# Kernel optimization log

Measured on AMD Instinct MI355X. Metric: run time of the kernel, lower is better.

Reference implementation:

```python
import jax, jax.numpy as jnp
import numpy as np

S, SM, B, D, H, NHEAD = 1024, 1024, 4, 1024, 2048, 16
EPS = 1e-5


def layer_norm(x, g, b):
    mu = jnp.mean(x, axis=-1, keepdims=True)
    var = jnp.var(x, axis=-1, keepdims=True)
    return (x - mu) * jax.lax.rsqrt(var + EPS) * g + b


def mha(q_in, k_in, v_in, w_in, b_in, w_out, b_out):
    # q_in: [Sq,B,D], k_in/v_in: [Sk,B,D]; torch nn.MultiheadAttention math (eval)
    Sq, Bn, Dn = q_in.shape
    Sk = k_in.shape[0]
    hd = Dn // NHEAD
    wq, wk, wv = jnp.split(w_in, 3, axis=0)
    bq, bk, bv = jnp.split(b_in, 3)
    q = (q_in @ wq.T + bq) * (hd ** -0.5)
    k = k_in @ wk.T + bk
    v = v_in @ wv.T + bv
    rs = lambda x, L: x.reshape(L, Bn, NHEAD, hd).transpose(1, 2, 0, 3)  # [B,h,L,hd]
    qh, kh, vh = rs(q, Sq), rs(k, Sk), rs(v, Sk)
    att = jax.nn.softmax(jnp.einsum('bhqd,bhkd->bhqk', qh, kh), axis=-1)
    o = jnp.einsum('bhqk,bhkd->bhqd', att, vh).transpose(2, 0, 1, 3).reshape(Sq, Bn, Dn)
    return o @ w_out.T + b_out


def sru(x, w, v, b):
    # SRU cell with input projection (n_in != n_out -> k=4): candidate, f, r, highway
    Ssz, Bsz, _ = x.shape
    U = (x @ w).reshape(Ssz, Bsz, 4, H)  # [S,B,4,H]
    vf, vr = v[0], v[1]
    bf, br = b[0], b[1]

    def step(c, u):
        xc, fp, rp, xh = u[:, 0], u[:, 1], u[:, 2], u[:, 3]
        f = jax.nn.sigmoid(fp + vf * c + bf)
        r = jax.nn.sigmoid(rp + vr * c + br)
        c2 = f * c + (1.0 - f) * xc
        h = r * c2 + (1.0 - r) * xh
        return c2, h

    c0 = jnp.zeros((Bsz, H), x.dtype)
    _, hs = jax.lax.scan(step, c0, U)
    return hs  # [S,B,H]


def setup_inputs():
    key = jax.random.key(0)
    ks = jax.random.split(key, 12)
    n = lambda k, shp, sc=0.02: jax.random.normal(k, shp, dtype=jnp.float32) * sc
    return dict(
        tgt=n(ks[0], (S, B, D), 1.0),
        memory=n(ks[1], (SM, B, D), 1.0),
        sa_w_in=n(ks[2], (3 * D, D)), sa_b_in=jnp.zeros((3 * D,)),
        sa_w_out=n(ks[3], (D, D)), sa_b_out=jnp.zeros((D,)),
        ca_w_in=n(ks[4], (3 * D, D)), ca_b_in=jnp.zeros((3 * D,)),
        ca_w_out=n(ks[5], (D, D)), ca_b_out=jnp.zeros((D,)),
        sru_w=n(ks[6], (D, 4 * H)), sru_v=n(ks[7], (2, H)), sru_b=jnp.zeros((2, H)),
        lin2_w=n(ks[8], (D, H)), lin2_b=jnp.zeros((D,)),
        ln1_g=jnp.ones((D,)), ln1_b=jnp.zeros((D,)),
        ln2_g=jnp.ones((D,)), ln2_b=jnp.zeros((D,)),
        ln3_g=jnp.ones((D,)), ln3_b=jnp.zeros((D,)),
    )


def reference(tgt, memory, sa_w_in, sa_b_in, sa_w_out, sa_b_out,
              ca_w_in, ca_b_in, ca_w_out, ca_b_out,
              sru_w, sru_v, sru_b, lin2_w, lin2_b,
              ln1_g, ln1_b, ln2_g, ln2_b, ln3_g, ln3_b):
    # dropout layers are identity in eval mode
    t2 = mha(tgt, tgt, tgt, sa_w_in, sa_b_in, sa_w_out, sa_b_out)
    t = layer_norm(tgt + t2, ln1_g, ln1_b)
    t2 = mha(t, memory, memory, ca_w_in, ca_b_in, ca_w_out, ca_b_out)
    t = layer_norm(t + t2, ln2_g, ln2_b)
    h = sru(t, sru_w, sru_v, sru_b)
    t2 = h @ lin2_w.T + lin2_b
    t = layer_norm(t + t2, ln3_g, ln3_b)
    return t
```

## Files before the change

kernel.cpp:

```cpp
#include <hip/hip_runtime.h>
#include <hip/hip_bf16.h>

typedef __bf16 bf16;
typedef bf16 bf16x8 __attribute__((ext_vector_type(8)));
typedef bf16 bf16x4 __attribute__((ext_vector_type(4)));
typedef float f32x4 __attribute__((ext_vector_type(4)));

#define MFMA16(a, b, c) __builtin_amdgcn_mfma_f32_16x16x32_bf16((a), (b), (c), 0, 0, 0)

__device__ __forceinline__ void gl_lds16(const void* g, void* l) {
    __builtin_amdgcn_global_load_lds((const __attribute__((address_space(1))) void*)g,
                                     (__attribute__((address_space(3))) void*)l, 16, 0, 0);
}

__global__ __launch_bounds__(256) void k_detect(const void* __restrict__ src, int* __restrict__ flag) {
    __shared__ int cnt;
    if (threadIdx.x == 0) cnt = 0;
    __syncthreads();
    const unsigned int* w = (const unsigned int*)src;
    int local = 0;
    for (int i = threadIdx.x; i < 4096; i += 256) {
        unsigned int e = (w[i] >> 7) & 0xFF;
        local += (e > 100 && e < 150) ? 1 : 0;
    }
    atomicAdd(&cnt, local);
    __syncthreads();
    if (threadIdx.x == 0) *flag = (cnt > 2048) ? 1 : 0;
}

struct BigSegs {
    const void* src[6];
    bf16* dst[6];
    int cum[7];
};
__global__ __launch_bounds__(256) void k_norm_big(const int* __restrict__ flag, BigSegs s) {
    if (*flag) return;
    int seg = 0;
#pragma unroll
    for (int t = 0; t < 5; t++) seg += (blockIdx.x >= s.cum[t + 1]) ? 1 : 0;
    int i = (blockIdx.x - s.cum[seg]) * 256 + threadIdx.x;
    const float* fs = (const float*)s.src[seg] + (size_t)i * 8;
    bf16x8 o;
#pragma unroll
    for (int j = 0; j < 8; j++) o[j] = (bf16)fs[j];
    ((bf16x8*)s.dst[seg])[i] = o;
}

struct SmallSegs {
    const void* src[13];
    bf16* dst[13];
    int n8[13];
};
__global__ __launch_bounds__(256) void k_norm_multi(const int* __restrict__ flag, SmallSegs s) {
    int seg = blockIdx.x;
    const void* sp = s.src[seg];
    bf16* dp = s.dst[seg];
    int n = s.n8[seg];
    int f = *flag;
    for (int i = threadIdx.x; i < n; i += 256) {
        if (f) {
            ((bf16x8*)dp)[i] = ((const bf16x8*)sp)[i];
        } else {
            const float* fs = (const float*)sp + (size_t)i * 8;
            bf16x8 o;
#pragma unroll
            for (int j = 0; j < 8; j++) o[j] = (bf16)fs[j];
            ((bf16x8*)dp)[i] = o;
        }
    }
}

__global__ __launch_bounds__(256) void k_cvt(const int* __restrict__ flag, const void* __restrict__ in,
                                             bf16* __restrict__ outb) {
    if (*flag) return;
    size_t i = (size_t)blockIdx.x * 256 + threadIdx.x;
    f32x4 a = ((const f32x4*)in)[i * 2];
    f32x4 b = ((const f32x4*)in)[i * 2 + 1];
    bf16x8 v;
#pragma unroll
    for (int j = 0; j < 4; j++) { v[j] = (bf16)a[j]; v[4 + j] = (bf16)b[j]; }
    ((bf16x8*)outb)[i] = v;
}

__global__ __launch_bounds__(256) void k_transpose(const int* __restrict__ flag, const void* __restrict__ in,
                                                   bf16* __restrict__ out, int R, int C) {
    __shared__ __align__(16) bf16 t[64][72];
    int tid = threadIdx.x;
    int c0 = blockIdx.x * 64, r0 = blockIdx.y * 64;
#pragma unroll
    for (int i = 0; i < 2; i++) {
        int idx = tid + i * 256;
        int r = idx >> 3, ch = idx & 7;
        size_t base = (size_t)(r0 + r) * C + c0 + ch * 8;
        bf16x8 v;
        if (*flag) {
            v = *(const bf16x8*)((const bf16*)in + base);
        } else {
            const float* f = (const float*)in + base;
            f32x4 x = *(const f32x4*)f, y = *(const f32x4*)(f + 4);
#pragma unroll
            for (int j = 0; j < 4; j++) { v[j] = (bf16)x[j]; v[4 + j] = (bf16)y[j]; }
        }
        *(bf16x8*)&t[r][ch * 8] = v;
    }
    __syncthreads();
    int nbase = c0 & 2047, joff = c0 >> 11;
#pragma unroll
    for (int i = 0; i < 2; i++) {
        int idx = tid + i * 256;
        int cr = idx >> 3, ch = idx & 7;
        bf16x8 v;
#pragma unroll
        for (int j = 0; j < 8; j++) v[j] = t[ch * 8 + j][cr];
        int np = (nbase + cr) * 4 + joff;
        *(bf16x8*)(out + (size_t)np * R + r0 + ch * 8) = v;
    }
}

__global__ __launch_bounds__(256) void k_vtr(const bf16* __restrict__ in, int ldv, bf16* __restrict__ out) {
    int nt = blockIdx.x, st = blockIdx.y, b = blockIdx.z;
    __shared__ __align__(16) bf16 t[64][72];
    int tid = threadIdx.x;
#pragma unroll
    for (int i = 0; i < 2; i++) {
        int idx = tid + i * 256;
        int r = idx >> 3, ch = idx & 7;
        bf16x8 v = *(const bf16x8*)(in + (size_t)((st * 64 + r) * 4 + b) * ldv + nt * 64 + ch * 8);
        *(bf16x8*)&t[r][ch * 8] = v;
    }
    __syncthreads();
#pragma unroll
    for (int i = 0; i < 2; i++) {
        int idx = tid + i * 256;
        int dr = idx >> 3, ch = idx & 7;
        bf16x8 v;
#pragma unroll
        for (int j = 0; j < 8; j++) v[j] = t[ch * 8 + j][dr];
        *(bf16x8*)(out + (size_t)(b * 1024 + nt * 64 + dr) * 1024 + st * 64 + ch * 8) = v;
    }
}

__device__ __forceinline__ int swzB(int r, int byteInRow) {
    return r * 128 + (byteInRow ^ ((r & 7) << 4));
}

template <int BM, bool USCAT>
__global__ __launch_bounds__(256) void k_gemm(
    const int* __restrict__ flagp,
    const bf16* __restrict__ A, const bf16* __restrict__ Aalt, int lda,
    const bf16* __restrict__ W, const bf16* __restrict__ Walt, int ldw,
    const bf16* __restrict__ bias,
    float* __restrict__ Cf, bf16* __restrict__ Cb, int ldc,
    int K, int scale_end, float scale) {
    constexpr int MI = BM / 32;
    __shared__ __align__(16) char Asm[BM * 128];
    __shared__ __align__(16) char Bsm[128 * 128];
    if (*flagp) {
        if (Aalt) A = Aalt;
        if (Walt) W = Walt;
    }
    int tid = threadIdx.x, w = tid >> 6, l = tid & 63, lg = l >> 4, lm = l & 15;
    int wm = w >> 1, wn = w & 1;
    int m0 = blockIdx.y * BM, n0 = blockIdx.x * 128;

    f32x4 acc[MI][4] = {};

    for (int k0 = 0; k0 < K; k0 += 64) {
#pragma unroll
        for (int i = 0; i < BM / 32; i++) {
            int r = i * 32 + w * 8 + (l >> 3);
            int gs = (l & 7) ^ (r & 7);
            gl_lds16(A + (size_t)(m0 + r) * lda + k0 + gs * 8,
                     Asm + (i * 32 + w * 8) * 128);
        }
#pragma unroll
        for (int i = 0; i < 4; i++) {
            int r = i * 32 + w * 8 + (l >> 3);
            int gs = (l & 7) ^ (r & 7);
            gl_lds16(W + (size_t)(n0 + r) * ldw + k0 + gs * 8,
                     Bsm + (i * 32 + w * 8) * 128);
        }
        __syncthreads();
#pragma unroll
        for (int kh = 0; kh < 2; kh++) {
            bf16x8 af[MI], bfr[4];
#pragma unroll
            for (int i = 0; i < MI; i++)
                af[i] = *(const bf16x8*)(Asm + swzB(wm * (BM / 2) + i * 16 + lm, kh * 64 + lg * 16));
#pragma unroll
            for (int j = 0; j < 4; j++)
                bfr[j] = *(const bf16x8*)(Bsm + swzB(wn * 64 + j * 16 + lm, kh * 64 + lg * 16));
#pragma unroll
            for (int i = 0; i < MI; i++)
#pragma unroll
                for (int j = 0; j < 4; j++)
                    acc[i][j] = MFMA16(af[i], bfr[j], acc[i][j]);
        }
        __syncthreads();
    }
    if constexpr (USCAT) {
        bf16* lsA = (bf16*)Asm;
        bf16* lsB = (bf16*)Bsm;
#pragma unroll
        for (int j = 0; j < 4; j++) {
            int cl = wn * 16 + j * 4 + (lm >> 2);
            int g = lm & 3;
            bf16* ls = (g < 2) ? lsA : lsB;
            int g01 = g & 1;
#pragma unroll
            for (int i = 0; i < MI; i++) {
                int slb = wm * 16 + i * 4 + lg;
                int boff = (slb * 2 + g01) * 2;
                int swz = boff ^ ((cl & 7) << 4);
#pragma unroll
                for (int r = 0; r < 4; r++) {
                    float v = acc[i][j][r];
                    *(bf16*)((char*)ls + (r * 32 + cl) * 128 + swz) = (bf16)v;
                }
            }
        }
        __syncthreads();
        int buf = tid >> 7, bb = (tid >> 5) & 3, cl = tid & 31;
        const char* ls = (buf == 0) ? (const char*)lsA : (const char*)lsB;
        bf16* dstbase = (buf == 0) ? Cb : (bf16*)Cf;
        int ch = bb * 2048 + (n0 >> 2) + cl;
        size_t gbase = (size_t)ch * 2048 + (size_t)(m0 >> 2) * 2;
        const char* src = ls + (bb * 32 + cl) * 128;
#pragma unroll
        for (int q = 0; q < 8; q++) {
            int pq = (q * 16) ^ ((cl & 7) << 4);
            *(bf16x8*)(dstbase + gbase + q * 8) = *(const bf16x8*)(src + pq);
        }
    } else {
#pragma unroll
        for (int j = 0; j < 4; j++) {
            int col = n0 + wn * 64 + j * 16 + lm;
            float bv = bias ? (float)bias[col] : 0.f;
            float sc = (col < scale_end) ? scale : 1.f;
#pragma unroll
            for (int i = 0; i < MI; i++) {
                int row = m0 + wm * (BM / 2) + i * 16 + lg * 4;
#pragma unroll
                for (int r = 0; r < 4; r++) {
                    float v = (acc[i][j][r] + bv) * sc;
                    size_t idx = (size_t)(row + r) * ldc + col;
                    if (Cf) Cf[idx] = v;
                    if (Cb) Cb[idx] = (bf16)v;
                }
            }
        }
    }
}

__device__ __forceinline__ int swz2(int row, int byteInRow) {
    return row * 128 + (byteInRow ^ ((row & 7) << 4));
}
__device__ __forceinline__ int swzP(int row, int byteInRow) {
    return row * 128 + (byteInRow ^ ((row & 3) << 4) ^ (((row >> 2) & 1) << 6));
}

__global__ __launch_bounds__(256) void k_attn(
    const bf16* __restrict__ Qp, const bf16* __restrict__ Kp, const bf16* __restrict__ Vt,
    int ldq, int ldk, bf16* __restrict__ Op) {
    int h = blockIdx.x & 15, b = blockIdx.x >> 4, qblk = blockIdx.y;
    int tid = threadIdx.x, w = tid >> 6, l = tid & 63, lg = l >> 4, lm = l & 15;
    int r0 = tid >> 3, ch = tid & 7;

    __shared__ __align__(16) char Ksm[2][64 * 128];
    __shared__ __align__(16) char Vsm[2][64 * 128];
    __shared__ __align__(16) char Psm[4][32 * 128];

    bf16x8 qf[2][2];
#pragma unroll
    for (int u = 0; u < 2; u++) {
        int qrow = qblk * 128 + w * 32 + u * 16 + lm;
#pragma unroll
        for (int kk = 0; kk < 2; kk++)
            qf[u][kk] = *(const bf16x8*)(Qp + (size_t)(qrow * 4 + b) * ldq + h * 64 + kk * 32 + lg * 8);
    }

    const bf16* vbase = Vt + (size_t)(b * 1024 + h * 64) * 1024;

    bf16x8 kreg[2], vreg[2];
#pragma unroll
    for (int p = 0; p < 2; p++) {
        int r = r0 + p * 32;
        kreg[p] = *(const bf16x8*)(Kp + (size_t)(r * 4 + b) * ldk + h * 64 + ch * 8);
        vreg[p] = *(const bf16x8*)(vbase + (size_t)r * 1024 + ch * 8);
    }
#pragma unroll
    for (int p = 0; p < 2; p++) {
        int r = r0 + p * 32;
        *(bf16x8*)(Ksm[0] + swz2(r, ch * 16)) = kreg[p];
        *(bf16x8*)(Vsm[0] + swz2(r, ch * 16)) = vreg[p];
    }
    __syncthreads();

    f32x4 oa[2][4] = {};
    float mrun[2][4], lrun[2][4];
#pragma unroll
    for (int u = 0; u < 2; u++)
#pragma unroll
        for (int r = 0; r < 4; r++) { mrun[u][r] = -1e30f; lrun[u][r] = 0.f; }

    int cur = 0;
    for (int kt = 0; kt < 16; kt++) {
        if (kt < 15) {
#pragma unroll
            for (int p = 0; p < 2; p++) {
                int r = (kt + 1) * 64 + r0 + p * 32;
                kreg[p] = *(const bf16x8*)(Kp + (size_t)(r * 4 + b) * ldk + h * 64 + ch * 8);
                vreg[p] = *(const bf16x8*)(vbase + (size_t)(r0 + p * 32) * 1024 + (kt + 1) * 64 + ch * 8);
            }
        }
        const char* Kc = Ksm[cur];
        const char* Vc = Vsm[cur];

        f32x4 sc[2][4] = {};
#pragma unroll
        for (int kk = 0; kk < 2; kk++)
#pragma unroll
            for (int jt = 0; jt < 4; jt++) {
                bf16x8 bk = *(const bf16x8*)(Kc + swz2(jt * 16 + lm, kk * 64 + lg * 16));
#pragma unroll
                for (int u = 0; u < 2; u++)
                    sc[u][jt] = MFMA16(qf[u][kk], bk, sc[u][jt]);
            }

        float lmax[2][4];
        bool grow = false;
#pragma unroll
        for (int u = 0; u < 2; u++)
#pragma unroll
            for (int r = 0; r < 4; r++) {
                lmax[u][r] = fmaxf(fmaxf(sc[u][0][r], sc[u][1][r]), fmaxf(sc[u][2][r], sc[u][3][r]));
                grow = grow || (lmax[u][r] > mrun[u][r] + 8.f);
            }
        if (__any(grow)) {
#pragma unroll
            for (int u = 0; u < 2; u++)
#pragma unroll
                for (int r = 0; r < 4; r++) {
                    float m = lmax[u][r];
#pragma unroll
                    for (int d = 1; d < 16; d <<= 1) m = fmaxf(m, __shfl_xor(m, d));
                    float mn = fmaxf(mrun[u][r], m);
                    float al = __expf(mrun[u][r] - mn);
                    mrun[u][r] = mn;
                    lrun[u][r] *= al;
#pragma unroll
                    for (int ot = 0; ot < 4; ot++) oa[u][ot][r] *= al;
                }
        }
#pragma unroll
        for (int u = 0; u < 2; u++)
#pragma unroll
            for (int jt = 0; jt < 4; jt++)
#pragma unroll
                for (int r = 0; r < 4; r++) {
                    float p = __expf(sc[u][jt][r] - mrun[u][r]);
                    sc[u][jt][r] = p;
                    lrun[u][r] += p;
                }
#pragma unroll
        for (int u = 0; u < 2; u++)
#pragma unroll
            for (int jt = 0; jt < 4; jt++)
#pragma unroll
                for (int r = 0; r < 4; r++)
                    *(bf16*)(Psm[w] + swzP(u * 16 + lg * 4 + r, (jt * 16 + lm) * 2)) = (bf16)sc[u][jt][r];
        asm volatile("s_waitcnt lgkmcnt(0)" ::: "memory");
        __builtin_amdgcn_sched_barrier(0);
#pragma unroll
        for (int kk = 0; kk < 2; kk++) {
            bf16x8 pa[2];
#pragma unroll
            for (int u = 0; u < 2; u++)
                pa[u] = *(const bf16x8*)(Psm[w] + swzP(u * 16 + lm, kk * 64 + lg * 16));
#pragma unroll
            for (int ot = 0; ot < 4; ot++) {
                bf16x8 bv = *(const bf16x8*)(Vc + swz2(ot * 16 + lm, kk * 64 + lg * 16));
#pragma unroll
                for (int u = 0; u < 2; u++)
                    oa[u][ot] = MFMA16(pa[u], bv, oa[u][ot]);
            }
        }
        if (kt < 15) {
            char* Kn = Ksm[cur ^ 1];
            char* Vn = Vsm[cur ^ 1];
#pragma unroll
            for (int p = 0; p < 2; p++) {
                int r = r0 + p * 32;
                *(bf16x8*)(Kn + swz2(r, ch * 16)) = kreg[p];
                *(bf16x8*)(Vn + swz2(r, ch * 16)) = vreg[p];
            }
            __syncthreads();
        }
        cur ^= 1;
    }
#pragma unroll
    for (int u = 0; u < 2; u++)
#pragma unroll
        for (int r = 0; r < 4; r++) {
#pragma unroll
            for (int d = 1; d < 16; d <<= 1) lrun[u][r] += __shfl_xor(lrun[u][r], d);
            float inv = 1.f / lrun[u][r];
            int srow = qblk * 128 + w * 32 + u * 16 + lg * 4 + r;
#pragma unroll
            for (int ot = 0; ot < 4; ot++) {
                int col = h * 64 + ot * 16 + lm;
                Op[(size_t)(srow * 4 + b) * 1024 + col] = (bf16)(oa[u][ot][r] * inv);
            }
        }
}

template <typename XT>
__global__ __launch_bounds__(256) void k_addln(
    const int* __restrict__ flagp,
    const XT* __restrict__ X, const XT* __restrict__ Xalt, const float* __restrict__ Yd,
    const bf16* __restrict__ g, const bf16* __restrict__ bb,
    float* __restrict__ outF, bf16* __restrict__ outB) {
    if (*flagp && Xalt) X = Xalt;
    int row = blockIdx.x * 4 + (threadIdx.x >> 6);
    int l = threadIdx.x & 63;
    const XT* xr = X + (size_t)row * 1024;
    const float* yr = Yd + (size_t)row * 1024;
    float v[16];
    float s = 0.f, s2 = 0.f;
#pragma unroll
    for (int q = 0; q < 4; q++) {
        float xa[4];
        if constexpr (sizeof(XT) == 4) {
            f32x4 a = *(const f32x4*)(xr + l * 4 + q * 256);
#pragma unroll
            for (int j = 0; j < 4; j++) xa[j] = a[j];
        } else {
            bf16x4 a = *(const bf16x4*)(xr + l * 4 + q * 256);
#pragma unroll
            for (int j = 0; j < 4; j++) xa[j] = (float)a[j];
        }
        f32x4 c = *(const f32x4*)(yr + l * 4 + q * 256);
#pragma unroll
        for (int j = 0; j < 4; j++) {
            float t = xa[j] + c[j];
            v[q * 4 + j] = t;
            s += t;
            s2 += t * t;
        }
    }
#pragma unroll
    for (int d = 1; d < 64; d <<= 1) { s += __shfl_xor(s, d); s2 += __shfl_xor(s2, d); }
    float mu = s * (1.f / 1024.f);
    float var = s2 * (1.f / 1024.f) - mu * mu;
    float rstd = rsqrtf(var + 1e-5f);
#pragma unroll
    for (int q = 0; q < 4; q++)
#pragma unroll
        for (int j = 0; j < 4; j++) {
            int col = l * 4 + q * 256 + j;
            float y = (v[q * 4 + j] - mu) * rstd * (float)g[col] + (float)bb[col];
            if (outF) outF[(size_t)row * 1024 + col] = y;
            if (outB) outB[(size_t)row * 1024 + col] = (bf16)y;
        }
}

__global__ __launch_bounds__(64) void k_sru_ab(
    const bf16* __restrict__ U2a, const bf16* __restrict__ v2, const bf16* __restrict__ b2,
    float* __restrict__ AB) {
    int ch = blockIdx.x * 64 + threadIdx.x;
    int g = blockIdx.y;
    int hh = ch & 2047;
    float vf = (float)v2[hh], bfv = (float)b2[hh];
    const bf16x8* u = (const bf16x8*)(U2a + (size_t)ch * 2048 + g * 256);
    float A = 1.f, c = 0.f;
    bf16x8 q[4];
#pragma unroll
    for (int i = 0; i < 4; i++) q[i] = u[i];
    for (int it = 0; it < 8; it++) {
#pragma unroll
        for (int j = 0; j < 4; j++) {
            int cidx = it * 4 + j;
            bf16x8 v = q[j];
            if (cidx + 4 < 32) q[j] = u[cidx + 4];
#pragma unroll
            for (int t = 0; t < 4; t++) {
                float xc = (float)v[t * 2], fp = (float)v[t * 2 + 1];
                float f = 1.f / (1.f + __expf(-(fp + vf * c + bfv)));
                A *= f;
                c = f * c + (1.f - f) * xc;
            }
        }
    }
    AB[(size_t)(g * 8192 + ch) * 2] = A;
    AB[(size_t)(g * 8192 + ch) * 2 + 1] = c;
}

__global__ __launch_bounds__(64) void k_sru_h(
    const bf16* __restrict__ U2a, const bf16* __restrict__ U2b,
    const bf16* __restrict__ v2, const bf16* __restrict__ b2,
    const float* __restrict__ AB, bf16* __restrict__ Hb) {
    int ch = blockIdx.x * 64 + threadIdx.x;
    int g = blockIdx.y;
    int b = ch >> 11, hh = ch & 2047;
    float vf = (float)v2[hh], vr = (float)v2[2048 + hh];
    float bfv = (float)b2[hh], brv = (float)b2[2048 + hh];
    float c = 0.f;
    for (int s = 0; s < g; s++) {
        float As = AB[(size_t)(s * 8192 + ch) * 2];
        float Bs = AB[(size_t)(s * 8192 + ch) * 2 + 1];
        c = As * c + Bs;
    }
    const bf16x8* ua = (const bf16x8*)(U2a + (size_t)ch * 2048 + g * 256);
    const bf16x8* ub = (const bf16x8*)(U2b + (size_t)ch * 2048 + g * 256);
    bf16* ho = Hb + ((size_t)(g * 128) * 4 + b) * 2048 + hh;
    bf16x8 qa[4], qb[4];
#pragma unroll
    for (int i = 0; i < 4; i++) { qa[i] = ua[i]; qb[i] = ub[i]; }
    for (int it = 0; it < 8; it++) {
#pragma unroll
        for (int j = 0; j < 4; j++) {
            int cidx = it * 4 + j;
            bf16x8 va = qa[j], vb = qb[j];
            if (cidx + 4 < 32) { qa[j] = ua[cidx + 4]; qb[j] = ub[cidx + 4]; }
#pragma unroll
            for (int t = 0; t < 4; t++) {
                float xc = (float)va[t * 2], fp = (float)va[t * 2 + 1];
                float rp = (float)vb[t * 2], xh = (float)vb[t * 2 + 1];
                float f = 1.f / (1.f + __expf(-(fp + vf * c + bfv)));
                float r = 1.f / (1.f + __expf(-(rp + vr * c + brv)));
                c = f * c + (1.f - f) * xc;
                float hv = r * c + (1.f - r) * xh;
                ho[(size_t)(cidx * 4 + t) * 8192] = (bf16)hv;
            }
        }
    }
}

extern "C" void kernel_launch(void* const* d_in, const int* in_sizes, int n_in,
                              void* d_out, int out_size, void* d_ws, size_t ws_size,
                              hipStream_t stream) {
    const size_t MB = 1u << 20;
    char* ws = (char*)d_ws;

    bf16* memB    = (bf16*)(ws + 0);
    bf16* sawinB  = (bf16*)(ws + 8 * MB);
    bf16* sawoutB = (bf16*)(ws + 14 * MB);
    bf16* cawinB  = (bf16*)(ws + 16 * MB);
    bf16* cawoutB = (bf16*)(ws + 22 * MB);
    bf16* lin2wB  = (bf16*)(ws + 24 * MB);
    char* S0 = ws + 28 * MB;
    bf16* sabinB  = (bf16*)(S0 + 0 * 8192);
    bf16* cabinB  = (bf16*)(S0 + 1 * 8192);
    bf16* saboutB = (bf16*)(S0 + 2 * 8192);
    bf16* caboutB = (bf16*)(S0 + 3 * 8192);
    bf16* lin2bB  = (bf16*)(S0 + 4 * 8192);
    bf16* sruvB   = (bf16*)(S0 + 5 * 8192);
    bf16* srubB   = (bf16*)(S0 + 6 * 8192);
    bf16* ln1gB   = (bf16*)(S0 + 7 * 8192);
    bf16* ln1bB   = (bf16*)(S0 + 8 * 8192);
    bf16* ln2gB   = (bf16*)(S0 + 9 * 8192);
    bf16* ln2bB   = (bf16*)(S0 + 10 * 8192);
    bf16* ln3gB   = (bf16*)(S0 + 11 * 8192);
    bf16* ln3bB   = (bf16*)(S0 + 12 * 8192);
    int*  flag    = (int*)(S0 + 13 * 8192);
    float* AB     = (float*)(S0 + 128 * 1024);

    char* P = ws + 29 * MB;
    bf16*  t0b  = (bf16*)(P + 0);
    bf16*  qkv  = (bf16*)(P + 16 * MB);
    bf16*  qca  = qkv;
    bf16*  kvca = (bf16*)(P + 24 * MB);
    bf16*  obuf = (bf16*)(P + 40 * MB);
    bf16*  Vt   = (bf16*)(P + 56 * MB);
    float* tmp  = (float*)(P + 64 * MB);
    bf16*  t1   = (bf16*)(P + 80 * MB);
    bf16*  t2   = (bf16*)(ws + 0);
    bf16*  wT   = (bf16*)(P + 0);
    bf16*  U2a  = (bf16*)(P + 16 * MB);
    bf16*  U2b  = (bf16*)(P + 48 * MB);
    bf16*  hb   = (bf16*)(P + 80 * MB);
    float* tmp2 = (float*)(P + 16 * MB);

    const bf16* tgtA   = (const bf16*)d_in[0];
    const bf16* memA   = (const bf16*)d_in[1];
    const bf16* sawinA = (const bf16*)d_in[2];
    const bf16* sawoutA= (const bf16*)d_in[4];
    const bf16* cawinA = (const bf16*)d_in[6];
    const bf16* cawoutA= (const bf16*)d_in[8];
    const bf16* lin2wA = (const bf16*)d_in[13];

    k_detect<<<1, 256, 0, stream>>>(d_in[0], flag);
    BigSegs bg;
    {
        const void* bsrc[6] = {d_in[1], d_in[2], d_in[4], d_in[6], d_in[8], d_in[13]};
        bf16* bdst[6] = {memB, sawinB, sawoutB, cawinB, cawoutB, lin2wB};
        const int cum[7] = {0, 2048, 3584, 4096, 5632, 6144, 7168};
        for (int i = 0; i < 6; i++) { bg.src[i] = bsrc[i]; bg.dst[i] = bdst[i]; }
        for (int i = 0; i < 7; i++) bg.cum[i] = cum[i];
    }
    k_norm_big<<<7168, 256, 0, stream>>>(flag, bg);
    SmallSegs sg;
    const int srcIdx[13] = {3, 7, 5, 9, 14, 11, 12, 15, 16, 17, 18, 19, 20};
    bf16* dsts[13] = {sabinB, cabinB, saboutB, caboutB, lin2bB, sruvB, srubB,
                      ln1gB, ln1bB, ln2gB, ln2bB, ln3gB, ln3bB};
    const int n8s[13] = {384, 384, 128, 128, 128, 512, 512, 128, 128, 128, 128, 128, 128};
    for (int i = 0; i < 13; i++) { sg.src[i] = d_in[srcIdx[i]]; sg.dst[i] = dsts[i]; sg.n8[i] = n8s[i]; }
    k_norm_multi<<<13, 256, 0, stream>>>(flag, sg);

    k_cvt<<<2048, 256, 0, stream>>>(flag, d_in[0], t0b);

    k_gemm<128, false><<<dim3(24, 32), 256, 0, stream>>>(flag, t0b, tgtA, 1024, sawinB, sawinA, 1024,
                                                         sabinB, nullptr, qkv, 3072, 1024, 1024, 0.125f);
    k_vtr<<<dim3(16, 16, 4), 256, 0, stream>>>(qkv + 2048, 3072, Vt);
    k_attn<<<dim3(64, 8), 256, 0, stream>>>(qkv, qkv + 1024, Vt, 3072, 3072, obuf);
    k_gemm<64, false><<<dim3(8, 64), 256, 0, stream>>>(flag, obuf, nullptr, 1024, sawoutB, sawoutA, 1024,
                                                       saboutB, tmp, nullptr, 1024, 1024, 0, 1.f);
    k_addln<bf16><<<1024, 256, 0, stream>>>(flag, t0b, tgtA, tmp, ln1gB, ln1bB, nullptr, t1);

    k_gemm<64, false><<<dim3(8, 64), 256, 0, stream>>>(flag, t1, nullptr, 1024, cawinB, cawinA, 1024,
                                                       cabinB, nullptr, qca, 1024, 1024, 1024, 0.125f);
    k_gemm<128, false><<<dim3(16, 32), 256, 0, stream>>>(flag, memB, memA, 1024,
                                                         cawinB + (size_t)1024 * 1024,
                                                         cawinA + (size_t)1024 * 1024, 1024,
                                                         cabinB + 1024, nullptr, kvca, 2048, 1024, 0, 1.f);
    k_vtr<<<dim3(16, 16, 4), 256, 0, stream>>>(kvca + 1024, 2048, Vt);
    k_attn<<<dim3(64, 8), 256, 0, stream>>>(qca, kvca, Vt, 1024, 2048, obuf);
    k_gemm<64, false><<<dim3(8, 64), 256, 0, stream>>>(flag, obuf, nullptr, 1024, cawoutB, cawoutA, 1024,
                                                       caboutB, tmp, nullptr, 1024, 1024, 0, 1.f);
    k_addln<bf16><<<1024, 256, 0, stream>>>(flag, t1, nullptr, tmp, ln2gB, ln2bB, nullptr, t2);

    k_transpose<<<dim3(128, 16), 256, 0, stream>>>(flag, d_in[10], wT, 1024, 8192);
    k_gemm<128, true><<<dim3(64, 32), 256, 0, stream>>>(flag, t2, nullptr, 1024, wT, nullptr, 1024,
                                                        nullptr, (float*)U2b, U2a, 0, 1024, 0, 1.f);
    k_sru_ab<<<dim3(128, 8), 64, 0, stream>>>(U2a, sruvB, srubB, AB);
    k_sru_h<<<dim3(128, 8), 64, 0, stream>>>(U2a, U2b, sruvB, srubB, AB, hb);
    k_gemm<64, false><<<dim3(8, 64), 256, 0, stream>>>(flag, hb, nullptr, 2048, lin2wB, lin2wA, 2048,
                                                       lin2bB, tmp2, nullptr, 1024, 2048, 0, 1.f);
    k_addln<bf16><<<1024, 256, 0, stream>>>(flag, t2, nullptr, tmp2, ln3gB, ln3bB, (float*)d_out, nullptr);
}
```

Baseline: 455.1 us.

## Use 256-row 512-thread GEMM for SRU projection and single-buffer attention K/V

Replaces the SRU input-projection GEMM (scatter-output variant) with a dedicated kernel using 256x128 tiles and 512 threads, so each A/W tile load feeds more MFMAs. The scatter epilogue now writes the two output buffers in two LDS passes. Separately, attention drops K/V double buffering in favour of a single LDS buffer with two barriers per iteration, which reduces LDS use and may raise occupancy but removes the overlap between the next tile's LDS store and compute.

```diff
diff --git a/kernel.cpp b/kernel.cpp
--- a/kernel.cpp
+++ b/kernel.cpp
@@ -144,7 +144,7 @@
     return r * 128 + (byteInRow ^ ((r & 7) << 4));
 }
 
-template <int BM, bool USCAT>
+template <int BM>
 __global__ __launch_bounds__(256) void k_gemm(
     const int* __restrict__ flagp,
     const bf16* __restrict__ A, const bf16* __restrict__ Aalt, int lda,
@@ -198,56 +198,104 @@
         }
         __syncthreads();
     }
-    if constexpr (USCAT) {
-        bf16* lsA = (bf16*)Asm;
-        bf16* lsB = (bf16*)Bsm;
-#pragma unroll
-        for (int j = 0; j < 4; j++) {
-            int cl = wn * 16 + j * 4 + (lm >> 2);
-            int g = lm & 3;
-            bf16* ls = (g < 2) ? lsA : lsB;
-            int g01 = g & 1;
-#pragma unroll
-            for (int i = 0; i < MI; i++) {
-                int slb = wm * 16 + i * 4 + lg;
-                int boff = (slb * 2 + g01) * 2;
-                int swz = boff ^ ((cl & 7) << 4);
-#pragma unroll
-                for (int r = 0; r < 4; r++) {
-                    float v = acc[i][j][r];
-                    *(bf16*)((char*)ls + (r * 32 + cl) * 128 + swz) = (bf16)v;
+#pragma unroll
+    for (int j = 0; j < 4; j++) {
+        int col = n0 + wn * 64 + j * 16 + lm;
+        float bv = bias ? (float)bias[col] : 0.f;
+        float sc = (col < scale_end) ? scale : 1.f;
+#pragma unroll
+        for (int i = 0; i < MI; i++) {
+            int row = m0 + wm * (BM / 2) + i * 16 + lg * 4;
+#pragma unroll
+            for (int r = 0; r < 4; r++) {
+                float v = (acc[i][j][r] + bv) * sc;
+                size_t idx = (size_t)(row + r) * ldc + col;
+                if (Cf) Cf[idx] = v;
+                if (Cb) Cb[idx] = (bf16)v;
+            }
+        }
+    }
+}
+
+__global__ __launch_bounds__(512) void k_gemm256u(
+    const bf16* __restrict__ A, int lda,
+    const bf16* __restrict__ W, int ldw,
+    bf16* __restrict__ U2a, bf16* __restrict__ U2b) {
+    __shared__ __align__(16) char Asm[256 * 128];
+    __shared__ __align__(16) char Bsm[128 * 128];
+    int tid = threadIdx.x, w = tid >> 6, l = tid & 63, lg = l >> 4, lm = l & 15;
+    int wm = w >> 1, wn = w & 1;
+    int m0 = blockIdx.y * 256, n0 = blockIdx.x * 128;
+
+    f32x4 acc[4][4] = {};
+
+    for (int k0 = 0; k0 < 1024; k0 += 64) {
+#pragma unroll
+        for (int i = 0; i < 4; i++) {
+            int r = i * 64 + w * 8 + (l >> 3);
+            int gs = (l & 7) ^ (r & 7);
+            gl_lds16(A + (size_t)(m0 + r) * lda + k0 + gs * 8,
+                     Asm + (i * 64 + w * 8) * 128);
+        }
+#pragma unroll
+        for (int i = 0; i < 2; i++) {
+            int r = i * 64 + w * 8 + (l >> 3);
+            int gs = (l & 7) ^ (r & 7);
+            gl_lds16(W + (size_t)(n0 + r) * ldw + k0 + gs * 8,
+                     Bsm + (i * 64 + w * 8) * 128);
+        }
+        __syncthreads();
+#pragma unroll
+        for (int kh = 0; kh < 2; kh++) {
+            bf16x8 af[4], bfr[4];
+#pragma unroll
+            for (int i = 0; i < 4; i++)
+                af[i] = *(const bf16x8*)(Asm + swzB(wm * 64 + i * 16 + lm, kh * 64 + lg * 16));
+#pragma unroll
+            for (int j = 0; j < 4; j++)
+                bfr[j] = *(const bf16x8*)(Bsm + swzB(wn * 64 + j * 16 + lm, kh * 64 + lg * 16));
+#pragma unroll
+            for (int i = 0; i < 4; i++)
+#pragma unroll
+                for (int j = 0; j < 4; j++)
+                    acc[i][j] = MFMA16(af[i], bfr[j], acc[i][j]);
+        }
+        __syncthreads();
+    }
+    bf16* ls = (bf16*)Asm;
+    int gate = lm & 3;
+    int g01 = gate & 1;
+    int mybuf = gate >> 1;
+#pragma unroll
+    for (int buf = 0; buf < 2; buf++) {
+        __syncthreads();
+        if (mybuf == buf) {
+#pragma unroll
+            for (int j = 0; j < 4; j++) {
+                int chl = wn * 16 + j * 4 + (lm >> 2);
+#pragma unroll
+                for (int i = 0; i < 4; i++) {
+                    int sl = wm * 16 + i * 4 + lg;
+                    int boff = (sl * 2 + g01) * 2;
+                    int swz = boff ^ ((chl & 7) << 4);
+#pragma unroll
+                    for (int r = 0; r < 4; r++)
+                        *(bf16*)((char*)ls + (r * 32 + chl) * 256 + swz) = (bf16)acc[i][j][r];
                 }
             }
         }
         __syncthreads();
-        int buf = tid >> 7, bb = (tid >> 5) & 3, cl = tid & 31;
-        const char* ls = (buf == 0) ? (const char*)lsA : (const char*)lsB;
-        bf16* dstbase = (buf == 0) ? Cb : (bf16*)Cf;
-        int ch = bb * 2048 + (n0 >> 2) + cl;
-        size_t gbase = (size_t)ch * 2048 + (size_t)(m0 >> 2) * 2;
-        const char* src = ls + (bb * 32 + cl) * 128;
-#pragma unroll
-        for (int q = 0; q < 8; q++) {
-            int pq = (q * 16) ^ ((cl & 7) << 4);
-            *(bf16x8*)(dstbase + gbase + q * 8) = *(const bf16x8*)(src + pq);
-        }
-    } else {
-#pragma unroll
-        for (int j = 0; j < 4; j++) {
-            int col = n0 + wn * 64 + j * 16 + lm;
-            float bv = bias ? (float)bias[col] : 0.f;
-            float sc = (col < scale_end) ? scale : 1.f;
-#pragma unroll
-            for (int i = 0; i < MI; i++) {
-                int row = m0 + wm * (BM / 2) + i * 16 + lg * 4;
-#pragma unroll
-                for (int r = 0; r < 4; r++) {
-                    float v = (acc[i][j][r] + bv) * sc;
-                    size_t idx = (size_t)(row + r) * ldc + col;
-                    if (Cf) Cf[idx] = v;
-                    if (Cb) Cb[idx] = (bf16)v;
-                }
-            }
+        int run = tid >> 2, part = tid & 3;
+        int bb = run >> 5, chl = run & 31;
+        bf16* dstb = (buf == 0) ? U2a : U2b;
+        int ch = bb * 2048 + (n0 >> 2) + chl;
+        size_t gb = (size_t)ch * 2048 + (size_t)(m0 >> 2) * 2;
+        const char* src = (const char*)ls + (bb * 32 + chl) * 256;
+#pragma unroll
+        for (int k = 0; k < 4; k++) {
+            int q = part * 4 + k;
+            int pq = (q * 16) ^ ((chl & 7) << 4);
+            *(bf16x8*)(dstb + gb + q * 8) = *(const bf16x8*)(src + pq);
         }
     }
 }
@@ -266,8 +314,8 @@
     int tid = threadIdx.x, w = tid >> 6, l = tid & 63, lg = l >> 4, lm = l & 15;
     int r0 = tid >> 3, ch = tid & 7;
 
-    __shared__ __align__(16) char Ksm[2][64 * 128];
-    __shared__ __align__(16) char Vsm[2][64 * 128];
+    __shared__ __align__(16) char Ksm[64 * 128];
+    __shared__ __align__(16) char Vsm[64 * 128];
     __shared__ __align__(16) char Psm[4][32 * 128];
 
     bf16x8 qf[2][2];
@@ -288,13 +336,6 @@
         kreg[p] = *(const bf16x8*)(Kp + (size_t)(r * 4 + b) * ldk + h * 64 + ch * 8);
         vreg[p] = *(const bf16x8*)(vbase + (size_t)r * 1024 + ch * 8);
     }
-#pragma unroll
-    for (int p = 0; p < 2; p++) {
-        int r = r0 + p * 32;
-        *(bf16x8*)(Ksm[0] + swz2(r, ch * 16)) = kreg[p];
-        *(bf16x8*)(Vsm[0] + swz2(r, ch * 16)) = vreg[p];
-    }
-    __syncthreads();
 
     f32x4 oa[2][4] = {};
     float mrun[2][4], lrun[2][4];
@@ -303,8 +344,14 @@
 #pragma unroll
         for (int r = 0; r < 4; r++) { mrun[u][r] = -1e30f; lrun[u][r] = 0.f; }
 
-    int cur = 0;
     for (int kt = 0; kt < 16; kt++) {
+        __syncthreads();
+#pragma unroll
+        for (int p = 0; p < 2; p++) {
+            int r = r0 + p * 32;
+            *(bf16x8*)(Ksm + swz2(r, ch * 16)) = kreg[p];
+            *(bf16x8*)(Vsm + swz2(r, ch * 16)) = vreg[p];
+        }
         if (kt < 15) {
 #pragma unroll
             for (int p = 0; p < 2; p++) {
@@ -313,15 +360,14 @@
                 vreg[p] = *(const bf16x8*)(vbase + (size_t)(r0 + p * 32) * 1024 + (kt + 1) * 64 + ch * 8);
             }
         }
-        const char* Kc = Ksm[cur];
-        const char* Vc = Vsm[cur];
+        __syncthreads();
 
         f32x4 sc[2][4] = {};
 #pragma unroll
         for (int kk = 0; kk < 2; kk++)
 #pragma unroll
             for (int jt = 0; jt < 4; jt++) {
-                bf16x8 bk = *(const bf16x8*)(Kc + swz2(jt * 16 + lm, kk * 64 + lg * 16));
+                bf16x8 bk = *(const bf16x8*)(Ksm + swz2(jt * 16 + lm, kk * 64 + lg * 16));
 #pragma unroll
                 for (int u = 0; u < 2; u++)
                     sc[u][jt] = MFMA16(qf[u][kk], bk, sc[u][jt]);
@@ -379,24 +425,12 @@
                 pa[u] = *(const bf16x8*)(Psm[w] + swzP(u * 16 + lm, kk * 64 + lg * 16));
 #pragma unroll
             for (int ot = 0; ot < 4; ot++) {
-                bf16x8 bv = *(const bf16x8*)(Vc + swz2(ot * 16 + lm, kk * 64 + lg * 16));
+                bf16x8 bv = *(const bf16x8*)(Vsm + swz2(ot * 16 + lm, kk * 64 + lg * 16));
 #pragma unroll
                 for (int u = 0; u < 2; u++)
                     oa[u][ot] = MFMA16(pa[u], bv, oa[u][ot]);
             }
         }
-        if (kt < 15) {
-            char* Kn = Ksm[cur ^ 1];
-            char* Vn = Vsm[cur ^ 1];
-#pragma unroll
-            for (int p = 0; p < 2; p++) {
-                int r = r0 + p * 32;
-                *(bf16x8*)(Kn + swz2(r, ch * 16)) = kreg[p];
-                *(bf16x8*)(Vn + swz2(r, ch * 16)) = vreg[p];
-            }
-            __syncthreads();
-        }
-        cur ^= 1;
     }
 #pragma unroll
     for (int u = 0; u < 2; u++)
@@ -609,32 +643,31 @@
 
     k_cvt<<<2048, 256, 0, stream>>>(flag, d_in[0], t0b);
 
-    k_gemm<128, false><<<dim3(24, 32), 256, 0, stream>>>(flag, t0b, tgtA, 1024, sawinB, sawinA, 1024,
-                                                         sabinB, nullptr, qkv, 3072, 1024, 1024, 0.125f);
+    k_gemm<128><<<dim3(24, 32), 256, 0, stream>>>(flag, t0b, tgtA, 1024, sawinB, sawinA, 1024,
+                                                  sabinB, nullptr, qkv, 3072, 1024, 1024, 0.125f);
     k_vtr<<<dim3(16, 16, 4), 256, 0, stream>>>(qkv + 2048, 3072, Vt);
     k_attn<<<dim3(64, 8), 256, 0, stream>>>(qkv, qkv + 1024, Vt, 3072, 3072, obuf);
-    k_gemm<64, false><<<dim3(8, 64), 256, 0, stream>>>(flag, obuf, nullptr, 1024, sawoutB, sawoutA, 1024,
-                                                       saboutB, tmp, nullptr, 1024, 1024, 0, 1.f);
+    k_gemm<64><<<dim3(8, 64), 256, 0, stream>>>(flag, obuf, nullptr, 1024, sawoutB, sawoutA, 1024,
+                                                saboutB, tmp, nullptr, 1024, 1024, 0, 1.f);
     k_addln<bf16><<<1024, 256, 0, stream>>>(flag, t0b, tgtA, tmp, ln1gB, ln1bB, nullptr, t1);
 
-    k_gemm<64, false><<<dim3(8, 64), 256, 0, stream>>>(flag, t1, nullptr, 1024, cawinB, cawinA, 1024,
-                                                       cabinB, nullptr, qca, 1024, 1024, 1024, 0.125f);
-    k_gemm<128, false><<<dim3(16, 32), 256, 0, stream>>>(flag, memB, memA, 1024,
-                                                         cawinB + (size_t)1024 * 1024,
-                                                         cawinA + (size_t)1024 * 1024, 1024,
-                                                         cabinB + 1024, nullptr, kvca, 2048, 1024, 0, 1.f);
+    k_gemm<64><<<dim3(8, 64), 256, 0, stream>>>(flag, t1, nullptr, 1024, cawinB, cawinA, 1024,
+                                                cabinB, nullptr, qca, 1024, 1024, 1024, 0.125f);
+    k_gemm<128><<<dim3(16, 32), 256, 0, stream>>>(flag, memB, memA, 1024,
+                                                  cawinB + (size_t)1024 * 1024,
+                                                  cawinA + (size_t)1024 * 1024, 1024,
+                                                  cabinB + 1024, nullptr, kvca, 2048, 1024, 0, 1.f);
     k_vtr<<<dim3(16, 16, 4), 256, 0, stream>>>(kvca + 1024, 2048, Vt);
     k_attn<<<dim3(64, 8), 256, 0, stream>>>(qca, kvca, Vt, 1024, 2048, obuf);
-    k_gemm<64, false><<<dim3(8, 64), 256, 0, stream>>>(flag, obuf, nullptr, 1024, cawoutB, cawoutA, 1024,
-                                                       caboutB, tmp, nullptr, 1024, 1024, 0, 1.f);
+    k_gemm<64><<<dim3(8, 64), 256, 0, stream>>>(flag, obuf, nullptr, 1024, cawoutB, cawoutA, 1024,
+                                                caboutB, tmp, nullptr, 1024, 1024, 0, 1.f);
     k_addln<bf16><<<1024, 256, 0, stream>>>(flag, t1, nullptr, tmp, ln2gB, ln2bB, nullptr, t2);
 
     k_transpose<<<dim3(128, 16), 256, 0, stream>>>(flag, d_in[10], wT, 1024, 8192);
-    k_gemm<128, true><<<dim3(64, 32), 256, 0, stream>>>(flag, t2, nullptr, 1024, wT, nullptr, 1024,
-                                                        nullptr, (float*)U2b, U2a, 0, 1024, 0, 1.f);
+    k_gemm256u<<<dim3(64, 16), 512, 0, stream>>>(t2, 1024, wT, 1024, U2a, U2b);
     k_sru_ab<<<dim3(128, 8), 64, 0, stream>>>(U2a, sruvB, srubB, AB);
     k_sru_h<<<dim3(128, 8), 64, 0, stream>>>(U2a, U2b, sruvB, srubB, AB, hb);
-    k_gemm<64, false><<<dim3(8, 64), 256, 0, stream>>>(flag, hb, nullptr, 2048, lin2wB, lin2wA, 2048,
-                                                       lin2bB, tmp2, nullptr, 1024, 2048, 0, 1.f);
+    k_gemm<64><<<dim3(8, 64), 256, 0, stream>>>(flag, hb, nullptr, 2048, lin2wB, lin2wA, 2048,
+                                                lin2bB, tmp2, nullptr, 1024, 2048, 0, 1.f);
     k_addln<bf16><<<1024, 256, 0, stream>>>(flag, t2, nullptr, tmp2, ln3gB, ln3bB, (float*)d_out, nullptr);
 }
```

Result: slower. 476.8 us (+4.8%).
